# Kernel optimization log

Hardware: AMD Instinct MI355X
Metric: run time of the kernel (lower is better)

The kernel has to match this reference:

```python
import jax, jax.numpy as jnp
import numpy as np
from jax import lax

KERNEL_SIZE = 11
DATA_RANGE = 1603.64208984375 - 1396.9390869140625


def build_gauss_kernel(size=11, sigma=1.0, n_channels=1):
    # Faithful replication of the torch helper (including its quirks):
    # gaussian(x) = exp((x-c)^2 / (-2 sigma^2)) ** 2, and the kernel is the
    # SUM of the two coordinate gaussians (np.sum over axis=2), normalized.
    grid = np.float32(np.mgrid[0:size, 0:size].T)  # (size, size, 2)

    def gaussian(x):
        return np.exp((x - size // 2) ** 2 / (-2 * sigma ** 2)) ** 2

    kernel = np.sum(gaussian(grid), axis=2)
    kernel /= np.sum(kernel)
    kernel = np.tile(kernel, (n_channels, 1, 1))  # (C, size, size)
    return jnp.asarray(kernel[:, None, :, :], dtype=jnp.float32)  # (C,1,k,k)


def _dwconv(x, w, pad):
    # depthwise conv, NCHW / OIHW, groups = channels (here 1)
    return lax.conv_general_dilated(
        x, w, window_strides=(1, 1), padding=[(pad, pad), (pad, pad)],
        dimension_numbers=("NCHW", "OIHW", "NCHW"),
        feature_group_count=x.shape[1])


def setup_inputs() -> dict:
    key = jax.random.key(0)
    k1, k2 = jax.random.split(key)
    B, C, H, W = 32, 1, 512, 512
    preds = jax.random.normal(k1, (B, C, H, W), dtype=jnp.float32)
    target = jax.random.normal(k2, (B, C, H, W), dtype=jnp.float32)
    window = build_gauss_kernel(KERNEL_SIZE, sigma=1.0, n_channels=C)
    return {"preds": preds, "target": target, "window": window}


def reference(preds, target, window):
    img1 = preds.astype(jnp.float32)
    img2 = target.astype(jnp.float32)
    C1 = (0.01 * DATA_RANGE) ** 2
    C2 = (0.03 * DATA_RANGE) ** 2
    pad = KERNEL_SIZE // 2

    mu1 = _dwconv(img1, window, pad)
    mu2 = _dwconv(img2, window, pad)
    mu1_sq = mu1 * mu1
    mu2_sq = mu2 * mu2
    mu1_mu2 = mu1 * mu2
    sigma1_sq = _dwconv(img1 * img1, window, pad) - mu1_sq
    sigma2_sq = _dwconv(img2 * img2, window, pad) - mu2_sq
    sigma12 = _dwconv(img1 * img2, window, pad) - mu1_mu2

    ssim_map = ((2 * mu1_mu2 + C1) * (2 * sigma12 + C2)) / (
        (mu1_sq + mu2_sq + C1) * (sigma1_sq + sigma2_sq + C2))
    return ssim_map.mean()  # average=True
```

## Files before the change

kernel.cpp:

```cpp
#include <hip/hip_runtime.h>


#define TH 16
#define TW 64
#define ICOLS 74
#define IS 76
#define VUNITS (ICOLS * 4)
#define NBLOCKS 8192

__device__ __forceinline__ float rfl_f32(float x) {
    return __uint_as_float(
        (unsigned)__builtin_amdgcn_readfirstlane((int)__float_as_uint(x)));
}

__device__ __forceinline__ unsigned pack_pair(float g, float b) {
    unsigned r;
    asm("v_cvt_pk_bf16_f32 %0, %1, %2" : "=v"(r) : "v"(b), "v"(g));
    return r;
}

__global__ __launch_bounds__(256, 4) void ssim_kernel(
    const float* __restrict__ x1, const float* __restrict__ x2,
    const float* __restrict__ win, float* __restrict__ part)
{
    __shared__ __align__(16) unsigned sp[5][TH][IS];
    __shared__ float partials[4];

    const int tid = threadIdx.x;
    const int tile_c0 = blockIdx.x * TW;
    const int tile_r0 = blockIdx.y * TH;
    const float* __restrict__ img1 = x1 + (size_t)blockIdx.z * (512 * 512);
    const float* __restrict__ img2 = x2 + (size_t)blockIdx.z * (512 * 512);

    float u[11];
    {
        float u0 = rfl_f32(win[0]) * 0.5f;
#pragma unroll
        for (int i = 0; i < 11; ++i)
            u[i] = (i == 0) ? u0 : (rfl_f32(win[i * 11]) - u0);
    }

    auto mathstore = [&](int rr0, int c, const float* V1, const float* V2) {
        float bx[5];
        float dd[3][5];
        float gg[4][5];
#pragma unroll
        for (int ch = 0; ch < 5; ++ch) {
            bx[ch] = 0.f;
#pragma unroll
            for (int j = 0; j < 3; ++j) dd[j][ch] = 0.f;
#pragma unroll
            for (int r = 0; r < 4; ++r) gg[r][ch] = 0.f;
        }
#pragma unroll
        for (int k = 0; k < 14; ++k) {
            float v1 = V1[k], v2 = V2[k];
            float p[5];
            p[0] = v1; p[1] = v2;
            p[2] = v1 * v1; p[3] = v2 * v2; p[4] = v1 * v2;
            if (k < 11) {
#pragma unroll
                for (int ch = 0; ch < 5; ++ch) bx[ch] += p[ch];
            }
            if (k < 3) {
#pragma unroll
                for (int ch = 0; ch < 5; ++ch) dd[k][ch] = -p[ch];
            }
            if (k >= 11) {
#pragma unroll
                for (int ch = 0; ch < 5; ++ch) dd[k - 11][ch] += p[ch];
            }
#pragma unroll
            for (int r = 0; r < 4; ++r) {
                if (k >= r + 4 && k <= r + 6) {
                    float w = u[k - r];
#pragma unroll
                    for (int ch = 0; ch < 5; ++ch)
                        gg[r][ch] = fmaf(w, p[ch], gg[r][ch]);
                }
            }
        }
#pragma unroll
        for (int r = 0; r < 4; ++r) {
#pragma unroll
            for (int ch = 0; ch < 5; ++ch)
                sp[ch][rr0 + r][c] = pack_pair(gg[r][ch], bx[ch]);
            if (r < 3) {
#pragma unroll
                for (int ch = 0; ch < 5; ++ch) bx[ch] += dd[r][ch];
            }
        }
    };

    const bool interior = (blockIdx.y >= 1) && (blockIdx.y <= 30) &&
                          (blockIdx.x >= 1) && (blockIdx.x <= 6);

    if (interior) {
        for (int unit = tid; unit < VUNITS; unit += 256) {
            int seg = unit / ICOLS, c = unit - seg * ICOLS, rr0 = seg * 4;
            const float* q1 = img1 + (tile_r0 + rr0 - 5) * 512 + (tile_c0 + c - 5);
            const float* q2 = img2 + (tile_r0 + rr0 - 5) * 512 + (tile_c0 + c - 5);
            float V1[14], V2[14];
#pragma unroll
            for (int k = 0; k < 14; ++k) { V1[k] = q1[k * 512]; V2[k] = q2[k * 512]; }
            mathstore(rr0, c, V1, V2);
        }
    } else {
        for (int unit = tid; unit < VUNITS; unit += 256) {
            int seg = unit / ICOLS, c = unit - seg * ICOLS, rr0 = seg * 4;
            int gc = tile_c0 + c - 5;
            int gr0 = tile_r0 + rr0 - 5;
            float V1[14], V2[14];
            if (((unsigned)gc < 512u) && ((unsigned)gr0 <= 498u)) {
                const float* q1 = img1 + gr0 * 512 + gc;
                const float* q2 = img2 + gr0 * 512 + gc;
#pragma unroll
                for (int k = 0; k < 14; ++k) { V1[k] = q1[k * 512]; V2[k] = q2[k * 512]; }
            } else {
                int gcc = min(max(gc, 0), 511);
                float mc = ((unsigned)gc < 512u) ? 1.0f : 0.0f;
#pragma unroll
                for (int k = 0; k < 14; ++k) {
                    int gr = gr0 + k;
                    int grc = min(max(gr, 0), 511);
                    float m = ((unsigned)gr < 512u) ? mc : 0.0f;
                    int off = grc * 512 + gcc;
                    V1[k] = img1[off] * m;
                    V2[k] = img2[off] * m;
                }
            }
            mathstore(rr0, c, V1, V2);
        }
    }
    __syncthreads();

    float local = 0.0f;
    {
        int r = tid >> 4;
        int cg = (tid & 15) * 4;

        float conv[5][4];
#pragma unroll
        for (int ch = 0; ch < 5; ++ch) {
            const uint4* p = (const uint4*)&sp[ch][r][cg];
            uint4 w0 = p[0], w1 = p[1], w2 = p[2];
            unsigned wc = ((const unsigned*)&sp[ch][r][cg])[12];
            unsigned wd = ((const unsigned*)&sp[ch][r][cg])[13];

            float gv[14], bv[10];
            gv[0]  = __uint_as_float(w0.x);
            gv[1]  = __uint_as_float(w0.y);
            gv[2]  = __uint_as_float(w0.z);
            gv[3]  = __uint_as_float(w0.w);
            gv[4]  = __uint_as_float(w1.x);
            gv[5]  = __uint_as_float(w1.y);
            gv[6]  = __uint_as_float(w1.z);
            gv[7]  = __uint_as_float(w1.w);
            gv[8]  = __uint_as_float(w2.x);
            gv[9]  = __uint_as_float(w2.y);
            gv[10] = __uint_as_float(w2.z);
            gv[11] = __uint_as_float(w2.w);
            gv[12] = __uint_as_float(wc);
            gv[13] = __uint_as_float(wd);
            bv[4]  = __uint_as_float(w1.x << 16);
            bv[5]  = __uint_as_float(w1.y << 16);
            bv[6]  = __uint_as_float(w1.z << 16);
            bv[7]  = __uint_as_float(w1.w << 16);
            bv[8]  = __uint_as_float(w2.x << 16);
            bv[9]  = __uint_as_float(w2.y << 16);

            float hs = 0.f;
#pragma unroll
            for (int j = 0; j < 11; ++j) hs += gv[j];
#pragma unroll
            for (int k = 0; k < 4; ++k) {
                float gs = u[4] * bv[k + 4];
                gs = fmaf(u[5], bv[k + 5], gs);
                gs = fmaf(u[6], bv[k + 6], gs);
                conv[ch][k] = hs + gs;
                if (k < 3) hs += gv[k + 11] - gv[k];
            }
        }

        constexpr double DR = 1603.64208984375 - 1396.9390869140625;
        constexpr float C1 = (float)((0.01 * DR) * (0.01 * DR));
        constexpr float C2 = (float)((0.03 * DR) * (0.03 * DR));
#pragma unroll
        for (int k = 0; k < 4; ++k) {
            float mu1 = conv[0][k], mu2 = conv[1][k];
            float e11 = conv[2][k], e22 = conv[3][k], e12 = conv[4][k];
            float mu1s = mu1 * mu1, mu2s = mu2 * mu2, mu12 = mu1 * mu2;
            float s1 = e11 - mu1s, s2 = e22 - mu2s, s12 = e12 - mu12;
            float num = (2.f * mu12 + C1) * (2.f * s12 + C2);
            float den = (mu1s + mu2s + C1) * (s1 + s2 + C2);
            local = fmaf(num, __builtin_amdgcn_rcpf(den), local);
        }
    }

#pragma unroll
    for (int off = 32; off > 0; off >>= 1) local += __shfl_down(local, off);
    if ((tid & 63) == 0) partials[tid >> 6] = local;
    __syncthreads();
    if (tid == 0) {
        int bidx = blockIdx.x + 8 * (blockIdx.y + 32 * blockIdx.z);
        part[bidx] = partials[0] + partials[1] + partials[2] + partials[3];
    }
}

__global__ __launch_bounds__(256) void reduce_kernel(
    const float* __restrict__ part, float* __restrict__ out)
{
    __shared__ float partials[4];
    float s = 0.0f;
    int tid = threadIdx.x;
    const float4* p4 = (const float4*)part;
#pragma unroll
    for (int i = 0; i < NBLOCKS / 1024; ++i) {
        float4 v = p4[tid + i * 256];
        s += (v.x + v.y) + (v.z + v.w);
    }
#pragma unroll
    for (int off = 32; off > 0; off >>= 1) s += __shfl_down(s, off);
    if ((tid & 63) == 0) partials[tid >> 6] = s;
    __syncthreads();
    if (tid == 0) {
        float t = partials[0] + partials[1] + partials[2] + partials[3];
        out[0] = t * (1.0f / 8388608.0f);
    }
}

extern "C" void kernel_launch(void* const* d_in, const int* in_sizes, int n_in,
                              void* d_out, int out_size, void* d_ws, size_t ws_size,
                              hipStream_t stream) {
    const float* preds  = (const float*)d_in[0];
    const float* target = (const float*)d_in[1];
    const float* window = (const float*)d_in[2];
    float* out = (float*)d_out;
    float* part = (float*)d_ws;

    dim3 grid(512 / TW, 512 / TH, 32);
    ssim_kernel<<<grid, 256, 0, stream>>>(preds, target, window, part);
    reduce_kernel<<<1, 256, 0, stream>>>(part, out);
}
```

Measured before the change: 120.6 us.

## Process four row tiles per block with software-prefetched next-tile loads

Each block now walks a band of four 16-row tiles in a loop, which cuts the grid to 2048 blocks and amortizes window setup across tiles. Inside the loop the global loads for the next tile's main units are issued into registers before the shared-memory convolution of the current tile, so load latency overlaps with compute. The cost is an extra barrier per tile, higher register pressure from the prefetch buffers, and fewer blocks to hide latency across the GPU.

```diff
diff --git a/kernel.cpp b/kernel.cpp
--- a/kernel.cpp
+++ b/kernel.cpp
@@ -6,7 +6,8 @@
 #define ICOLS 74
 #define IS 76
 #define VUNITS (ICOLS * 4)
-#define NBLOCKS 8192
+#define NTILES 4
+#define NBLOCKS 2048
 
 __device__ __forceinline__ float rfl_f32(float x) {
     return __uint_as_float(
@@ -28,7 +29,7 @@
 
     const int tid = threadIdx.x;
     const int tile_c0 = blockIdx.x * TW;
-    const int tile_r0 = blockIdx.y * TH;
+    const int band_r0 = blockIdx.y * (TH * NTILES);
     const float* __restrict__ img1 = x1 + (size_t)blockIdx.z * (512 * 512);
     const float* __restrict__ img2 = x2 + (size_t)blockIdx.z * (512 * 512);
 
@@ -92,109 +93,133 @@
         }
     };
 
-    const bool interior = (blockIdx.y >= 1) && (blockIdx.y <= 30) &&
-                          (blockIdx.x >= 1) && (blockIdx.x <= 6);
-
-    if (interior) {
-        for (int unit = tid; unit < VUNITS; unit += 256) {
-            int seg = unit / ICOLS, c = unit - seg * ICOLS, rr0 = seg * 4;
-            const float* q1 = img1 + (tile_r0 + rr0 - 5) * 512 + (tile_c0 + c - 5);
-            const float* q2 = img2 + (tile_r0 + rr0 - 5) * 512 + (tile_c0 + c - 5);
-            float V1[14], V2[14];
+    auto load_fast = [&](int tr0, int rr0, int c, float* V1, float* V2) {
+        const float* q1 = img1 + (tr0 + rr0 - 5) * 512 + (tile_c0 + c - 5);
+        const float* q2 = img2 + (tr0 + rr0 - 5) * 512 + (tile_c0 + c - 5);
+#pragma unroll
+        for (int k = 0; k < 14; ++k) { V1[k] = q1[k * 512]; V2[k] = q2[k * 512]; }
+    };
+    auto load_clamp = [&](int tr0, int rr0, int c, float* V1, float* V2) {
+        int gc = tile_c0 + c - 5;
+        int gr0 = tr0 + rr0 - 5;
+        if (((unsigned)gc < 512u) && ((unsigned)gr0 <= 498u)) {
+            const float* q1 = img1 + gr0 * 512 + gc;
+            const float* q2 = img2 + gr0 * 512 + gc;
 #pragma unroll
             for (int k = 0; k < 14; ++k) { V1[k] = q1[k * 512]; V2[k] = q2[k * 512]; }
-            mathstore(rr0, c, V1, V2);
-        }
-    } else {
-        for (int unit = tid; unit < VUNITS; unit += 256) {
-            int seg = unit / ICOLS, c = unit - seg * ICOLS, rr0 = seg * 4;
-            int gc = tile_c0 + c - 5;
-            int gr0 = tile_r0 + rr0 - 5;
-            float V1[14], V2[14];
-            if (((unsigned)gc < 512u) && ((unsigned)gr0 <= 498u)) {
-                const float* q1 = img1 + gr0 * 512 + gc;
-                const float* q2 = img2 + gr0 * 512 + gc;
-#pragma unroll
-                for (int k = 0; k < 14; ++k) { V1[k] = q1[k * 512]; V2[k] = q2[k * 512]; }
-            } else {
-                int gcc = min(max(gc, 0), 511);
-                float mc = ((unsigned)gc < 512u) ? 1.0f : 0.0f;
-#pragma unroll
-                for (int k = 0; k < 14; ++k) {
-                    int gr = gr0 + k;
-                    int grc = min(max(gr, 0), 511);
-                    float m = ((unsigned)gr < 512u) ? mc : 0.0f;
-                    int off = grc * 512 + gcc;
-                    V1[k] = img1[off] * m;
-                    V2[k] = img2[off] * m;
+        } else {
+            int gcc = min(max(gc, 0), 511);
+            float mc = ((unsigned)gc < 512u) ? 1.0f : 0.0f;
+#pragma unroll
+            for (int k = 0; k < 14; ++k) {
+                int gr = gr0 + k;
+                int grc = min(max(gr, 0), 511);
+                float m = ((unsigned)gr < 512u) ? mc : 0.0f;
+                int off = grc * 512 + gcc;
+                V1[k] = img1[off] * m;
+                V2[k] = img2[off] * m;
+            }
+        }
+    };
+
+    const bool colint = (blockIdx.x >= 1) && (blockIdx.x <= 6);
+
+    const int seg_m = tid / ICOLS;
+    const int c_m   = tid - seg_m * ICOLS;
+    const int rr0_m = seg_m * 4;
+    const bool has_tail = (tid < VUNITS - 256);
+    const int c_t = (VUNITS - 256 > 0) ? (256 - 3 * ICOLS + tid) : 0;
+
+    float P1[14], P2[14];
+    float local = 0.0f;
+
+#pragma unroll 1
+    for (int t = 0; t < NTILES; ++t) {
+        const int tr0 = band_r0 + t * TH;
+        const bool int_t = colint && (tr0 >= 5) && (tr0 <= 491);
+
+        if (t == 0 || !int_t) {
+            if (int_t) load_fast(tr0, rr0_m, c_m, P1, P2);
+            else       load_clamp(tr0, rr0_m, c_m, P1, P2);
+        }
+        mathstore(rr0_m, c_m, P1, P2);
+
+        if (t + 1 < NTILES) {
+            const int trn = tr0 + TH;
+            const bool int_n = colint && (trn >= 5) && (trn <= 491);
+            if (int_n) load_fast(trn, rr0_m, c_m, P1, P2);
+        }
+
+        if (has_tail) {
+            float T1[14], T2[14];
+            if (int_t) load_fast(tr0, 12, c_t, T1, T2);
+            else       load_clamp(tr0, 12, c_t, T1, T2);
+            mathstore(12, c_t, T1, T2);
+        }
+        __syncthreads();
+
+        {
+            int r = tid >> 4;
+            int cg = (tid & 15) * 4;
+
+            float conv[5][4];
+#pragma unroll
+            for (int ch = 0; ch < 5; ++ch) {
+                const uint4* p = (const uint4*)&sp[ch][r][cg];
+                uint4 w0 = p[0], w1 = p[1], w2 = p[2];
+                unsigned wc = ((const unsigned*)&sp[ch][r][cg])[12];
+                unsigned wd = ((const unsigned*)&sp[ch][r][cg])[13];
+
+                float gv[14], bv[10];
+                gv[0]  = __uint_as_float(w0.x);
+                gv[1]  = __uint_as_float(w0.y);
+                gv[2]  = __uint_as_float(w0.z);
+                gv[3]  = __uint_as_float(w0.w);
+                gv[4]  = __uint_as_float(w1.x);
+                gv[5]  = __uint_as_float(w1.y);
+                gv[6]  = __uint_as_float(w1.z);
+                gv[7]  = __uint_as_float(w1.w);
+                gv[8]  = __uint_as_float(w2.x);
+                gv[9]  = __uint_as_float(w2.y);
+                gv[10] = __uint_as_float(w2.z);
+                gv[11] = __uint_as_float(w2.w);
+                gv[12] = __uint_as_float(wc);
+                gv[13] = __uint_as_float(wd);
+                bv[4]  = __uint_as_float(w1.x << 16);
+                bv[5]  = __uint_as_float(w1.y << 16);
+                bv[6]  = __uint_as_float(w1.z << 16);
+                bv[7]  = __uint_as_float(w1.w << 16);
+                bv[8]  = __uint_as_float(w2.x << 16);
+                bv[9]  = __uint_as_float(w2.y << 16);
+
+                float hs = 0.f;
+#pragma unroll
+                for (int j = 0; j < 11; ++j) hs += gv[j];
+#pragma unroll
+                for (int k = 0; k < 4; ++k) {
+                    float gs = u[4] * bv[k + 4];
+                    gs = fmaf(u[5], bv[k + 5], gs);
+                    gs = fmaf(u[6], bv[k + 6], gs);
+                    conv[ch][k] = hs + gs;
+                    if (k < 3) hs += gv[k + 11] - gv[k];
                 }
             }
-            mathstore(rr0, c, V1, V2);
-        }
-    }
-    __syncthreads();
-
-    float local = 0.0f;
-    {
-        int r = tid >> 4;
-        int cg = (tid & 15) * 4;
-
-        float conv[5][4];
-#pragma unroll
-        for (int ch = 0; ch < 5; ++ch) {
-            const uint4* p = (const uint4*)&sp[ch][r][cg];
-            uint4 w0 = p[0], w1 = p[1], w2 = p[2];
-            unsigned wc = ((const unsigned*)&sp[ch][r][cg])[12];
-            unsigned wd = ((const unsigned*)&sp[ch][r][cg])[13];
-
-            float gv[14], bv[10];
-            gv[0]  = __uint_as_float(w0.x);
-            gv[1]  = __uint_as_float(w0.y);
-            gv[2]  = __uint_as_float(w0.z);
-            gv[3]  = __uint_as_float(w0.w);
-            gv[4]  = __uint_as_float(w1.x);
-            gv[5]  = __uint_as_float(w1.y);
-            gv[6]  = __uint_as_float(w1.z);
-            gv[7]  = __uint_as_float(w1.w);
-            gv[8]  = __uint_as_float(w2.x);
-            gv[9]  = __uint_as_float(w2.y);
-            gv[10] = __uint_as_float(w2.z);
-            gv[11] = __uint_as_float(w2.w);
-            gv[12] = __uint_as_float(wc);
-            gv[13] = __uint_as_float(wd);
-            bv[4]  = __uint_as_float(w1.x << 16);
-            bv[5]  = __uint_as_float(w1.y << 16);
-            bv[6]  = __uint_as_float(w1.z << 16);
-            bv[7]  = __uint_as_float(w1.w << 16);
-            bv[8]  = __uint_as_float(w2.x << 16);
-            bv[9]  = __uint_as_float(w2.y << 16);
-
-            float hs = 0.f;
-#pragma unroll
-            for (int j = 0; j < 11; ++j) hs += gv[j];
+
+            constexpr double DR = 1603.64208984375 - 1396.9390869140625;
+            constexpr float C1 = (float)((0.01 * DR) * (0.01 * DR));
+            constexpr float C2 = (float)((0.03 * DR) * (0.03 * DR));
 #pragma unroll
             for (int k = 0; k < 4; ++k) {
-                float gs = u[4] * bv[k + 4];
-                gs = fmaf(u[5], bv[k + 5], gs);
-                gs = fmaf(u[6], bv[k + 6], gs);
-                conv[ch][k] = hs + gs;
-                if (k < 3) hs += gv[k + 11] - gv[k];
-            }
-        }
-
-        constexpr double DR = 1603.64208984375 - 1396.9390869140625;
-        constexpr float C1 = (float)((0.01 * DR) * (0.01 * DR));
-        constexpr float C2 = (float)((0.03 * DR) * (0.03 * DR));
-#pragma unroll
-        for (int k = 0; k < 4; ++k) {
-            float mu1 = conv[0][k], mu2 = conv[1][k];
-            float e11 = conv[2][k], e22 = conv[3][k], e12 = conv[4][k];
-            float mu1s = mu1 * mu1, mu2s = mu2 * mu2, mu12 = mu1 * mu2;
-            float s1 = e11 - mu1s, s2 = e22 - mu2s, s12 = e12 - mu12;
-            float num = (2.f * mu12 + C1) * (2.f * s12 + C2);
-            float den = (mu1s + mu2s + C1) * (s1 + s2 + C2);
-            local = fmaf(num, __builtin_amdgcn_rcpf(den), local);
-        }
+                float mu1 = conv[0][k], mu2 = conv[1][k];
+                float e11 = conv[2][k], e22 = conv[3][k], e12 = conv[4][k];
+                float mu1s = mu1 * mu1, mu2s = mu2 * mu2, mu12 = mu1 * mu2;
+                float s1 = e11 - mu1s, s2 = e22 - mu2s, s12 = e12 - mu12;
+                float num = (2.f * mu12 + C1) * (2.f * s12 + C2);
+                float den = (mu1s + mu2s + C1) * (s1 + s2 + C2);
+                local = fmaf(num, __builtin_amdgcn_rcpf(den), local);
+            }
+        }
+        __syncthreads();
     }
 
 #pragma unroll
@@ -202,7 +227,7 @@
     if ((tid & 63) == 0) partials[tid >> 6] = local;
     __syncthreads();
     if (tid == 0) {
-        int bidx = blockIdx.x + 8 * (blockIdx.y + 32 * blockIdx.z);
+        int bidx = blockIdx.x + 8 * (blockIdx.y + 8 * blockIdx.z);
         part[bidx] = partials[0] + partials[1] + partials[2] + partials[3];
     }
 }
@@ -238,7 +263,7 @@
     float* out = (float*)d_out;
     float* part = (float*)d_ws;
 
-    dim3 grid(512 / TW, 512 / TH, 32);
+    dim3 grid(512 / TW, 512 / (TH * NTILES), 32);
     ssim_kernel<<<grid, 256, 0, stream>>>(preds, target, window, part);
     reduce_kernel<<<1, 256, 0, stream>>>(part, out);
 }
```

Result: slower. 124.9 us (+3.5%).
